# Optimization experiments

Hardware: AMD Instinct MI355X
Metric: run time of the kernel (lower is better)

Reference implementation:

```python
import jax, jax.numpy as jnp
import numpy as np

B, HIST, N, E = 16, 24, 256, 4096
AQI_EM, RNN_H, GNN_H, EDGE_H = 16, 64, 64, 2


def _lstm(x, W_ih, W_hh, b_ih, b_hh):
    # x: [Bn, L, in]; PyTorch LSTM cell, gate order i,f,g,o
    Bn, L, _ = x.shape
    H = W_hh.shape[1]
    xg = jnp.einsum('bli,gi->blg', x, W_ih) + b_ih  # precompute input contributions [Bn,L,4H]

    def step(carry, g_t):
        h, c = carry
        gates = g_t + h @ W_hh.T + b_hh
        i, f, g, o = jnp.split(gates, 4, axis=-1)
        c = jax.nn.sigmoid(f) * c + jax.nn.sigmoid(i) * jnp.tanh(g)
        h = jax.nn.sigmoid(o) * jnp.tanh(c)
        return (h, c), h

    init = (jnp.zeros((Bn, H), x.dtype), jnp.zeros((Bn, H), x.dtype))
    _, hs = jax.lax.scan(step, init, jnp.swapaxes(xg, 0, 1))
    return jnp.swapaxes(hs, 0, 1)  # [Bn,L,H]


def setup_inputs() -> dict:
    key = jax.random.key(0)
    ks = jax.random.split(key, 8)
    return {
        'city_aqi': jax.random.normal(ks[0], (B, HIST, N, 1), jnp.float32),
        'city_conn': jax.random.randint(ks[1], (2, E), 0, N, jnp.int32),
        'city_w': jax.random.normal(ks[2], (E, EDGE_H), jnp.float32),
        'embed_W': jax.random.normal(ks[3], (1, AQI_EM), jnp.float32) * 0.5,
        'embed_b': jnp.zeros((AQI_EM,), jnp.float32),
        'W_ih': jax.random.normal(ks[4], (4 * RNN_H, AQI_EM), jnp.float32) * (1.0 / np.sqrt(RNN_H)),
        'W_hh': jax.random.normal(ks[5], (4 * RNN_H, RNN_H), jnp.float32) * (1.0 / np.sqrt(RNN_H)),
        'b_ih': jnp.zeros((4 * RNN_H,), jnp.float32),
        'b_hh': jnp.zeros((4 * RNN_H,), jnp.float32),
        'mlp1_W': jax.random.normal(ks[6], (2 * RNN_H + EDGE_H, GNN_H), jnp.float32) * (1.0 / np.sqrt(2 * RNN_H + EDGE_H)),
        'mlp1_b': jnp.zeros((GNN_H,), jnp.float32),
        'mlp2_W': jax.random.normal(ks[7], (RNN_H + GNN_H, GNN_H), jnp.float32) * (1.0 / np.sqrt(RNN_H + GNN_H)),
        'mlp2_b': jnp.zeros((GNN_H,), jnp.float32),
        'city_num': N,
    }


def reference(city_aqi, city_conn, city_w, embed_W, embed_b, W_ih, W_hh, b_ih, b_hh, mlp1_W, mlp1_b, mlp2_W, mlp2_b, city_num):
    Bq, L, Nn, _ = city_aqi.shape
    # embedding + LSTM front-end
    x = jnp.transpose(city_aqi, (0, 2, 1, 3))          # [B,N,L,1]
    x = x @ embed_W + embed_b                          # [B,N,L,em]
    x = x.reshape(Bq * Nn, L, -1)
    h = _lstm(x, W_ih, W_hh, b_ih, b_hh)               # [B*N,L,H]
    h = jnp.transpose(h.reshape(Bq, Nn, L, -1), (0, 2, 1, 3))  # [B,L,N,H]
    # batched graph: T = B*L independent graphs with identical edge structure
    T = Bq * L
    x_flat = h.reshape(T * Nn, -1)                     # [T*N,H]
    off = jnp.arange(T, dtype=city_conn.dtype) * jnp.asarray(city_num, city_conn.dtype)
    row = (city_conn[0][None, :] + off[:, None]).reshape(-1)  # [T*E]
    col = (city_conn[1][None, :] + off[:, None]).reshape(-1)
    e = city_conn.shape[1]
    edge_attr = jnp.broadcast_to(city_w[None], (T, e, city_w.shape[1])).reshape(T * e, -1)
    # CityGNN: gather -> concat -> Linear -> scatter_mean -> concat -> Linear
    msg = jnp.concatenate([x_flat[row], x_flat[col], edge_attr], axis=1)
    msg = msg @ mlp1_W + mlp1_b                        # [T*E,gnn_h]
    agg = jax.ops.segment_sum(msg, col, num_segments=T * Nn)
    cnt = jax.ops.segment_sum(jnp.ones((T * e,), msg.dtype), col, num_segments=T * Nn)
    agg = agg / jnp.maximum(cnt, 1.0)[:, None]         # scatter_mean semantics
    out = jnp.concatenate([x_flat, agg], axis=1) @ mlp2_W + mlp2_b
    return out.reshape(-1, L, Nn, out.shape[-1])       # [B,hist_len,N,gnn_h]
```

## Files before the change

### kernel.cpp

```cpp
#include <hip/hip_runtime.h>
#include <hip/hip_bf16.h>

#define B_ 16
#define L_ 24
#define N_ 256
#define E_ 4096
#define T_ (B_ * L_)

constexpr int WP    = 0;
constexpr int WRQ   = WP + 4096;
constexpr int WRM   = WRQ + 4096;
constexpr int WBIAS = WRM + 4096;
constexpr int WALPHA= WBIAS + 16384;
constexpr int WBETA = WALPHA + 256;
constexpr int WDINV = WBETA + 256;
constexpr int WSEL  = WDINV + 256;
constexpr int WSW   = WSEL + 256;
constexpr int WCNTF = WSW + 512;
constexpr int WCOLP = WCNTF + 256;
constexpr int WROWS = WCOLP + 260;
constexpr int WHFRAG= WROWS + 4096;
constexpr int WQFRAG= WHFRAG + 8192;
constexpr int WX    = WQFRAG + 4096;
constexpr int WAFRG = WX + 3145728;

using bf16x8 = __attribute__((ext_vector_type(8))) short;
using f32x4  = __attribute__((ext_vector_type(4))) float;

__device__ __forceinline__ float rcp_(float x) { return __builtin_amdgcn_rcpf(x); }
__device__ __forceinline__ float sigm(float x) { return rcp_(1.f + __expf(-x)); }
__device__ __forceinline__ float tanh_(float x) {
    return fmaf(2.f, rcp_(1.f + __expf(-2.f * x)), -1.f);
}
__device__ __forceinline__ unsigned f2bf(float f) {
    unsigned u = __float_as_uint(f);
    return (u + 0x7fffu + ((u >> 16) & 1u)) >> 16;
}

constexpr int HS = 72;

__global__ __launch_bounds__(256, 1) void k_main(
    const float* __restrict__ aqi, const int* __restrict__ conn,
    const float* __restrict__ cw, const float* __restrict__ Wih,
    const float* __restrict__ embW, const float* __restrict__ embB,
    const float* __restrict__ bih, const float* __restrict__ bhh,
    const float* __restrict__ Whh, const float* __restrict__ m1W,
    const float* __restrict__ m1b, const float* __restrict__ m2W,
    const float* __restrict__ m2b, float* __restrict__ ws) {
    __shared__ __align__(16) char smem[65536];
    int t = threadIdx.x, blk = blockIdx.x;

    if (blk >= 256) {
        int role = blk - 256;
        if (role == 0) {
            int* s_cnt   = (int*)smem;
            float* s_sw0 = (float*)(smem + 1024);
            float* s_sw1 = (float*)(smem + 2048);
            float* sU    = (float*)(smem + 3072);
            s_cnt[t] = 0; s_sw0[t] = 0.f; s_sw1[t] = 0.f;
            __syncthreads();
            for (int e = t; e < E_; e += 256) {
                int c = conn[E_ + e] & 255;
                atomicAdd(&s_cnt[c], 1);
                atomicAdd(&s_sw0[c], cw[2 * e]);
                atomicAdd(&s_sw1[c], cw[2 * e + 1]);
            }
            __syncthreads();
            int cnt = s_cnt[t];
            ws[WCNTF + t] = (float)cnt;
            ws[WDINV + t] = 1.f / (float)(cnt > 1 ? cnt : 1);
            ws[WSEL + t]  = cnt > 0 ? 1.f : 0.f;
            ws[WSW + t]        = s_sw0[t];
            ws[WSW + N_ + t]   = s_sw1[t];
            if (t < 192) {
                int part = t >> 6, j = t & 63;
                float acc = 0.f;
                #pragma unroll 8
                for (int m = 0; m < 64; ++m) {
                    float w = (part == 0) ? m1W[128 * 64 + m]
                            : (part == 1) ? m1W[129 * 64 + m] : m1b[m];
                    acc = fmaf(w, m2W[(64 + m) * 64 + j], acc);
                }
                sU[part * 64 + j] = acc;
            }
            __syncthreads();
            {
                int j = t & 63;
                float u0 = sU[j], u1 = sU[64 + j], u2 = sU[128 + j];
                float b2j = m2b[j];
                int vb = t >> 6;
                #pragma unroll 8
                for (int i = 0; i < 64; ++i) {
                    int v = vb + i * 4;
                    int cv = s_cnt[v];
                    float dv = 1.f / (float)(cv > 1 ? cv : 1);
                    float bb = s_sw0[v] * u0 + s_sw1[v] * u1 + (float)cv * u2;
                    ws[WBIAS + v * 64 + j] = dv * bb + b2j;
                }
            }
            return;
        }
        if (role <= 4) {
            float* sB = (float*)smem;
            float* sM = (float*)(smem + 16384);
            int mi = role - 1;
            bool isP = mi < 2;
            int ks = mi & 1;
            #pragma unroll
            for (int i = 0; i < 16; ++i) sB[t + 256 * i] = m2W[64 * 64 + t + 256 * i];
            __syncthreads();
            int j = t & 63, kl = t >> 6;
            for (int r = 0; r < 8; ++r) {
                int kk = kl * 8 + r;
                int k = ks * 32 + kk;
                const float* arow = m1W + (isP ? k : (64 + k)) * 64;
                float acc = 0.f;
                #pragma unroll
                for (int m = 0; m < 64; m += 4) {
                    float4 a4 = *(const float4*)(arow + m);
                    acc = fmaf(a4.x, sB[m * 64 + j], acc);
                    acc = fmaf(a4.y, sB[(m + 1) * 64 + j], acc);
                    acc = fmaf(a4.z, sB[(m + 2) * 64 + j], acc);
                    acc = fmaf(a4.w, sB[(m + 3) * 64 + j], acc);
                }
                if (isP) {
                    sM[kk * 64 + j] = acc;
                } else {
                    ws[WRM + k * 64 + j] = acc;
                    sM[kk * 64 + j] = acc + m2W[k * 64 + j];
                }
            }
            __syncthreads();
            {
                int ct = t >> 6, l = t & 63;
                int fi = (isP ? 8 : 0) + ks * 4 + ct;
                int rb = (l >> 4) * 8;
                int n = ct * 16 + (l & 15);
                unsigned uu[4];
                #pragma unroll
                for (int q = 0; q < 4; ++q)
                    uu[q] = f2bf(sM[(rb + 2 * q) * 64 + n])
                          | (f2bf(sM[(rb + 2 * q + 1) * 64 + n]) << 16);
                ((uint4*)(ws + WQFRAG))[fi * 64 + l] = make_uint4(uu[0], uu[1], uu[2], uu[3]);
            }
            return;
        }
        unsigned* Mw = (unsigned*)smem;
        for (int i = t; i < 256 * 64; i += 256) Mw[i] = 0u;
        __syncthreads();
        for (int e = t; e < E_; e += 256) {
            int k = conn[e] & 255;
            int v = conn[E_ + e] & 255;
            atomicAdd(&Mw[v * 64 + (k >> 2)], 1u << ((k & 3) * 8));
        }
        __syncthreads();
        uint4* dst = (uint4*)(ws + WAFRG);
        int base = (role - 5) * 2048;
        #pragma unroll
        for (int u0 = 0; u0 < 8; ++u0) {
            int u = base + u0 * 256 + t;
            int fi = u >> 6, l = u & 63;
            int nt = fi >> 3, ks = fi & 7;
            int v = nt * 16 + (l & 15);
            int kb = ks * 8 + ((l >> 4) << 1);
            unsigned w0 = Mw[v * 64 + kb];
            unsigned w1 = Mw[v * 64 + kb + 1];
            unsigned uu[4];
            #pragma unroll
            for (int q = 0; q < 2; ++q) {
                unsigned c0 = (w0 >> (q * 16)) & 255u;
                unsigned c1 = (w0 >> (q * 16 + 8)) & 255u;
                uu[q] = f2bf((float)c0) | (f2bf((float)c1) << 16);
                unsigned d0 = (w1 >> (q * 16)) & 255u;
                unsigned d1 = (w1 >> (q * 16 + 8)) & 255u;
                uu[2 + q] = f2bf((float)d0) | (f2bf((float)d1) << 16);
            }
            dst[u] = make_uint4(uu[0], uu[1], uu[2], uu[3]);
        }
        return;
    }

    short* sHhi = (short*)smem;
    short* sHlo = (short*)(smem + 4608);
    float* sX   = (float*)(smem + 9216);
    int w = t >> 6, lane = t & 63;
    int seq0 = blk * 16;
    int b0 = seq0 >> 8, n0 = seq0 & 255;
    int c0 = lane & 15, quad = lane >> 4, q4 = quad * 4, q8 = quad * 8;
    bf16x8 wreg[4][2];
    #pragma unroll
    for (int g = 0; g < 4; ++g) {
        int ct = 4 * g + w;
        #pragma unroll
        for (int ks = 0; ks < 2; ++ks) {
            const float* src = Whh + (ct * 16 + c0) * 64 + ks * 32 + q8;
            union { bf16x8 v; unsigned u[4]; } tmp;
            #pragma unroll
            for (int q = 0; q < 4; ++q)
                tmp.u[q] = f2bf(src[2 * q]) | (f2bf(src[2 * q + 1]) << 16);
            wreg[g][ks] = tmp.v;
        }
    }
    for (int i = t; i < 384; i += 256) {
        int l = i >> 4, c = i & 15;
        sX[l * 16 + c] = aqi[(b0 * L_ + l) * N_ + n0 + c];
    }
    float alF[4][4], beF[4][4];
    #pragma unroll
    for (int g = 0; g < 4; ++g) {
        #pragma unroll
        for (int r = 0; r < 4; ++r) {
            int tp = (4 * g + w) * 16 + q4 + r;
            float a = 0.f, b = 0.f;
            #pragma unroll
            for (int i = 0; i < 16; ++i) {
                float wv = Wih[tp * 16 + i];
                a += wv * embW[i];
                b += wv * embB[i];
            }
            alF[g][r] = a;
            beF[g][r] = b + bih[tp] + bhh[tp];
        }
    }
    unsigned short* xws = (unsigned short*)(ws + WX);
    float cst[4] = {0.f, 0.f, 0.f, 0.f};
    bf16x8 hA[2][2] = {};
    __syncthreads();
    for (int l = 0; l < L_; ++l) {
        int buf = l & 1;
        float xv = sX[l * 16 + c0];
        f32x4 acc[4];
        #pragma unroll
        for (int g = 0; g < 4; ++g) {
            #pragma unroll
            for (int r = 0; r < 4; ++r)
                acc[g][r] = fmaf(xv, alF[g][r], beF[g][r]);
        }
        if (l > 0) {
            #pragma unroll
            for (int g = 0; g < 4; ++g) {
                #pragma unroll
                for (int ks = 0; ks < 2; ++ks) {
                    acc[g] = __builtin_amdgcn_mfma_f32_16x16x32_bf16(
                        wreg[g][ks], hA[0][ks], acc[g], 0, 0, 0);
                    acc[g] = __builtin_amdgcn_mfma_f32_16x16x32_bf16(
                        wreg[g][ks], hA[1][ks], acc[g], 0, 0, 0);
                }
            }
        }
        unsigned hb[4], lb[4];
        #pragma unroll
        for (int r = 0; r < 4; ++r) {
            float iv = sigm(acc[0][r]);
            float fv = sigm(acc[1][r]);
            float gv = tanh_(acc[2][r]);
            float ov = sigm(acc[3][r]);
            cst[r] = fmaf(fv, cst[r], iv * gv);
            float h = ov * tanh_(cst[r]);
            hb[r] = f2bf(h);
            float hf = __uint_as_float(hb[r] << 16);
            lb[r] = f2bf(h - hf);
        }
        uint2 hw = make_uint2(hb[0] | (hb[1] << 16), hb[2] | (hb[3] << 16));
        uint2 lw = make_uint2(lb[0] | (lb[1] << 16), lb[2] | (lb[3] << 16));
        *(uint2*)&sHhi[buf * (16 * HS) + c0 * HS + w * 16 + q4] = hw;
        *(uint2*)&sHlo[buf * (16 * HS) + c0 * HS + w * 16 + q4] = lw;
        *(uint2*)(xws + ((size_t)(b0 * L_ + l) * N_ + n0) * 64
                  + c0 * 64 + w * 16 + q4) = hw;
        asm volatile("s_waitcnt lgkmcnt(0)" ::: "memory");
        __builtin_amdgcn_s_barrier();
        hA[0][0] = *(const bf16x8*)&sHhi[buf * (16 * HS) + c0 * HS + q8];
        hA[0][1] = *(const bf16x8*)&sHhi[buf * (16 * HS) + c0 * HS + 32 + q8];
        hA[1][0] = *(const bf16x8*)&sHlo[buf * (16 * HS) + c0 * HS + q8];
        hA[1][1] = *(const bf16x8*)&sHlo[buf * (16 * HS) + c0 * HS + 32 + q8];
    }
}

constexpr int XS = 72;

__global__ __launch_bounds__(256, 2) void k_graph(
    const float* __restrict__ ws, float* __restrict__ out) {
    __shared__ __align__(16) short Xl[N_ * XS];
    __shared__ __align__(16) short Sl[N_ * XS];
    int tg = blockIdx.x;
    int tid = threadIdx.x;
    int lane = tid & 63, w = tid >> 6;
    int c0 = lane & 15, quad = lane >> 4, q8 = quad * 8;
    const uint4* src = (const uint4*)((const unsigned short*)(ws + WX)
                                      + (size_t)tg * (N_ * 64));
    #pragma unroll
    for (int it = 0; it < 8; ++it) {
        int idx = tid + it * 256;
        uint4 d = src[idx];
        int node = idx >> 3, q = idx & 7;
        *(uint4*)&Xl[node * XS + q * 8] = d;
    }
    float dv[16];
    #pragma unroll
    for (int nt = 0; nt < 16; ++nt) dv[nt] = ws[WDINV + nt * 16 + c0];
    __syncthreads();
    bf16x8 af[8];
    {
        int colb = w * 16 + (c0 & 14);
        int sh = (c0 & 1) * 16;
        int rbase = (lane >> 4) * 8;
        #pragma unroll
        for (int ks = 0; ks < 8; ++ks) {
            unsigned wd[8];
            #pragma unroll
            for (int j = 0; j < 8; ++j)
                wd[j] = *(const unsigned*)&Xl[(ks * 32 + rbase + j) * XS + colb];
            union { bf16x8 v; unsigned u[4]; } tmp;
            #pragma unroll
            for (int q = 0; q < 4; ++q)
                tmp.u[q] = ((wd[2 * q] >> sh) & 0xffffu)
                         | (((wd[2 * q + 1] >> sh) & 0xffffu) << 16);
            af[ks] = tmp.v;
        }
    }
    f32x4 acc[16];
    #pragma unroll
    for (int nt = 0; nt < 16; ++nt) {
        #pragma unroll
        for (int r = 0; r < 4; ++r) acc[nt][r] = 0.f;
    }
    {
        const bf16x8* bsrc = (const bf16x8*)(ws + WAFRG);
        #pragma unroll
        for (int nt = 0; nt < 16; ++nt) {
            bf16x8 bf[8];
            #pragma unroll
            for (int ks = 0; ks < 8; ++ks)
                bf[ks] = bsrc[(nt * 8 + ks) * 64 + lane];
            #pragma unroll
            for (int ks = 0; ks < 8; ++ks)
                acc[nt] = __builtin_amdgcn_mfma_f32_16x16x32_bf16(
                    af[ks], bf[ks], acc[nt], 0, 0, 0);
        }
    }
    {
        int j0 = w * 16 + quad * 4;
        #pragma unroll
        for (int nt = 0; nt < 16; ++nt) {
            float d = dv[nt];
            unsigned p0 = f2bf(acc[nt][0] * d) | (f2bf(acc[nt][1] * d) << 16);
            unsigned p1 = f2bf(acc[nt][2] * d) | (f2bf(acc[nt][3] * d) << 16);
            int v = nt * 16 + c0;
            *(uint2*)&Sl[v * XS + j0] = make_uint2(p0, p1);
        }
    }
    __syncthreads();
    bf16x8 bq[16];
    {
        const bf16x8* qf = (const bf16x8*)(ws + WQFRAG);
        #pragma unroll
        for (int i = 0; i < 16; ++i) bq[i] = qf[i * 64 + lane];
    }
    const float* bias = ws + WBIAS;
    #pragma unroll
    for (int rti = 0; rti < 4; ++rti) {
        int rt = w * 4 + rti;
        const short* xr = &Xl[(rt * 16 + c0) * XS];
        const short* sr = &Sl[(rt * 16 + c0) * XS];
        bf16x8 ax0 = *(const bf16x8*)(xr + q8);
        bf16x8 ax1 = *(const bf16x8*)(xr + 32 + q8);
        bf16x8 as0 = *(const bf16x8*)(sr + q8);
        bf16x8 as1 = *(const bf16x8*)(sr + 32 + q8);
        #pragma unroll
        for (int ct = 0; ct < 4; ++ct) {
            f32x4 a2;
            #pragma unroll
            for (int r = 0; r < 4; ++r)
                a2[r] = bias[(rt * 16 + quad * 4 + r) * 64 + ct * 16 + c0];
            a2 = __builtin_amdgcn_mfma_f32_16x16x32_bf16(ax0, bq[ct],      a2, 0, 0, 0);
            a2 = __builtin_amdgcn_mfma_f32_16x16x32_bf16(ax1, bq[4 + ct],  a2, 0, 0, 0);
            a2 = __builtin_amdgcn_mfma_f32_16x16x32_bf16(as0, bq[8 + ct],  a2, 0, 0, 0);
            a2 = __builtin_amdgcn_mfma_f32_16x16x32_bf16(as1, bq[12 + ct], a2, 0, 0, 0);
            #pragma unroll
            for (int r = 0; r < 4; ++r)
                out[((size_t)tg * 256 + rt * 16 + quad * 4 + r) * 64 + ct * 16 + c0]
                    = a2[r];
        }
    }
    int v = tid;
    float sel = ws[WSEL + v];
    if (__syncthreads_or(sel < 0.5f)) {
        if (sel < 0.5f) {
            float* og = out + ((size_t)tg * 256 + v) * 64;
            #pragma unroll
            for (int jc = 0; jc < 4; ++jc) {
                float corr[16];
                #pragma unroll
                for (int j = 0; j < 16; ++j) corr[j] = 0.f;
                #pragma unroll
                for (int k = 0; k < 64; ++k) {
                    unsigned hv = (unsigned short)Xl[v * XS + k];
                    float xk = __uint_as_float(hv << 16);
                    const float* Q = ws + WRM + k * 64 + jc * 16;
                    #pragma unroll
                    for (int j = 0; j < 16; ++j) corr[j] += xk * Q[j];
                }
                #pragma unroll
                for (int j = 0; j < 16; ++j) og[jc * 16 + j] -= corr[j];
            }
        }
    }
}

extern "C" void kernel_launch(void* const* d_in, const int* in_sizes, int n_in,
                              void* d_out, int out_size, void* d_ws, size_t ws_size,
                              hipStream_t stream) {
    const float* aqi  = (const float*)d_in[0];
    const int*   conn = (const int*)d_in[1];
    const float* cw   = (const float*)d_in[2];
    const float* embW = (const float*)d_in[3];
    const float* embB = (const float*)d_in[4];
    const float* Wih  = (const float*)d_in[5];
    const float* Whh  = (const float*)d_in[6];
    const float* bih  = (const float*)d_in[7];
    const float* bhh  = (const float*)d_in[8];
    const float* m1W  = (const float*)d_in[9];
    const float* m1b  = (const float*)d_in[10];
    const float* m2W  = (const float*)d_in[11];
    const float* m2b  = (const float*)d_in[12];
    float* ws  = (float*)d_ws;
    float* out = (float*)d_out;

    k_main<<<dim3(265), dim3(256), 0, stream>>>(aqi, conn, cw, Wih, embW, embB,
                                                bih, bhh, Whh, m1W, m1b, m2W,
                                                m2b, ws);
    k_graph<<<dim3(T_), dim3(256), 0, stream>>>(ws, out);
}
```

Measured before the change: 134.8 us.

## Process two 16-sequence LSTM tiles per block with interleaved recurrences

```diff
diff --git a/kernel.cpp b/kernel.cpp
--- a/kernel.cpp
+++ b/kernel.cpp
@@ -38,6 +38,7 @@
 }
 
 constexpr int HS = 72;
+constexpr int NLSTM = 128;
 
 __global__ __launch_bounds__(256, 1) void k_main(
     const float* __restrict__ aqi, const int* __restrict__ conn,
@@ -50,8 +51,8 @@
     __shared__ __align__(16) char smem[65536];
     int t = threadIdx.x, blk = blockIdx.x;
 
-    if (blk >= 256) {
-        int role = blk - 256;
+    if (blk >= NLSTM) {
+        int role = blk - NLSTM;
         if (role == 0) {
             int* s_cnt   = (int*)smem;
             float* s_sw0 = (float*)(smem + 1024);
@@ -180,11 +181,13 @@
         return;
     }
 
-    short* sHhi = (short*)smem;
-    short* sHlo = (short*)(smem + 4608);
-    float* sX   = (float*)(smem + 9216);
+    short* sHhiA = (short*)smem;
+    short* sHloA = (short*)(smem + 4608);
+    short* sHhiB = (short*)(smem + 9216);
+    short* sHloB = (short*)(smem + 13824);
+    float* sX    = (float*)(smem + 18432);
     int w = t >> 6, lane = t & 63;
-    int seq0 = blk * 16;
+    int seq0 = blk * 32;
     int b0 = seq0 >> 8, n0 = seq0 & 255;
     int c0 = lane & 15, quad = lane >> 4, q4 = quad * 4, q8 = quad * 8;
     bf16x8 wreg[4][2];
@@ -201,9 +204,9 @@
             wreg[g][ks] = tmp.v;
         }
     }
-    for (int i = t; i < 384; i += 256) {
-        int l = i >> 4, c = i & 15;
-        sX[l * 16 + c] = aqi[(b0 * L_ + l) * N_ + n0 + c];
+    for (int i = t; i < 768; i += 256) {
+        int l = i >> 5, c = i & 31;
+        sX[l * 32 + c] = aqi[(b0 * L_ + l) * N_ + n0 + c];
     }
     float alF[4][4], beF[4][4];
     #pragma unroll
@@ -223,56 +226,98 @@
         }
     }
     unsigned short* xws = (unsigned short*)(ws + WX);
-    float cst[4] = {0.f, 0.f, 0.f, 0.f};
-    bf16x8 hA[2][2] = {};
+    float cstA[4] = {0.f, 0.f, 0.f, 0.f};
+    float cstB[4] = {0.f, 0.f, 0.f, 0.f};
+    bf16x8 hAa[2][2] = {};
+    bf16x8 hAb[2][2] = {};
     __syncthreads();
     for (int l = 0; l < L_; ++l) {
         int buf = l & 1;
-        float xv = sX[l * 16 + c0];
-        f32x4 acc[4];
+        float xvA = sX[l * 32 + c0];
+        float xvB = sX[l * 32 + 16 + c0];
+        f32x4 accA[4], accB[4];
         #pragma unroll
         for (int g = 0; g < 4; ++g) {
             #pragma unroll
-            for (int r = 0; r < 4; ++r)
-                acc[g][r] = fmaf(xv, alF[g][r], beF[g][r]);
+            for (int r = 0; r < 4; ++r) {
+                accA[g][r] = fmaf(xvA, alF[g][r], beF[g][r]);
+                accB[g][r] = fmaf(xvB, alF[g][r], beF[g][r]);
+            }
         }
         if (l > 0) {
             #pragma unroll
             for (int g = 0; g < 4; ++g) {
                 #pragma unroll
                 for (int ks = 0; ks < 2; ++ks) {
-                    acc[g] = __builtin_amdgcn_mfma_f32_16x16x32_bf16(
-                        wreg[g][ks], hA[0][ks], acc[g], 0, 0, 0);
-                    acc[g] = __builtin_amdgcn_mfma_f32_16x16x32_bf16(
-                        wreg[g][ks], hA[1][ks], acc[g], 0, 0, 0);
-                }
-            }
-        }
-        unsigned hb[4], lb[4];
-        #pragma unroll
-        for (int r = 0; r < 4; ++r) {
-            float iv = sigm(acc[0][r]);
-            float fv = sigm(acc[1][r]);
-            float gv = tanh_(acc[2][r]);
-            float ov = sigm(acc[3][r]);
-            cst[r] = fmaf(fv, cst[r], iv * gv);
-            float h = ov * tanh_(cst[r]);
-            hb[r] = f2bf(h);
-            float hf = __uint_as_float(hb[r] << 16);
-            lb[r] = f2bf(h - hf);
-        }
-        uint2 hw = make_uint2(hb[0] | (hb[1] << 16), hb[2] | (hb[3] << 16));
-        uint2 lw = make_uint2(lb[0] | (lb[1] << 16), lb[2] | (lb[3] << 16));
-        *(uint2*)&sHhi[buf * (16 * HS) + c0 * HS + w * 16 + q4] = hw;
-        *(uint2*)&sHlo[buf * (16 * HS) + c0 * HS + w * 16 + q4] = lw;
-        *(uint2*)(xws + ((size_t)(b0 * L_ + l) * N_ + n0) * 64
-                  + c0 * 64 + w * 16 + q4) = hw;
+                    accA[g] = __builtin_amdgcn_mfma_f32_16x16x32_bf16(
+                        wreg[g][ks], hAa[0][ks], accA[g], 0, 0, 0);
+                    accA[g] = __builtin_amdgcn_mfma_f32_16x16x32_bf16(
+                        wreg[g][ks], hAa[1][ks], accA[g], 0, 0, 0);
+                }
+            }
+            #pragma unroll
+            for (int g = 0; g < 4; ++g) {
+                #pragma unroll
+                for (int ks = 0; ks < 2; ++ks) {
+                    accB[g] = __builtin_amdgcn_mfma_f32_16x16x32_bf16(
+                        wreg[g][ks], hAb[0][ks], accB[g], 0, 0, 0);
+                    accB[g] = __builtin_amdgcn_mfma_f32_16x16x32_bf16(
+                        wreg[g][ks], hAb[1][ks], accB[g], 0, 0, 0);
+                }
+            }
+        }
+        {
+            unsigned hb[4], lb[4];
+            #pragma unroll
+            for (int r = 0; r < 4; ++r) {
+                float iv = sigm(accA[0][r]);
+                float fv = sigm(accA[1][r]);
+                float gv = tanh_(accA[2][r]);
+                float ov = sigm(accA[3][r]);
+                cstA[r] = fmaf(fv, cstA[r], iv * gv);
+                float h = ov * tanh_(cstA[r]);
+                hb[r] = f2bf(h);
+                float hf = __uint_as_float(hb[r] << 16);
+                lb[r] = f2bf(h - hf);
+            }
+            uint2 hw = make_uint2(hb[0] | (hb[1] << 16), hb[2] | (hb[3] << 16));
+            uint2 lw = make_uint2(lb[0] | (lb[1] << 16), lb[2] | (lb[3] << 16));
+            *(uint2*)&sHhiA[buf * (16 * HS) + c0 * HS + w * 16 + q4] = hw;
+            *(uint2*)&sHloA[buf * (16 * HS) + c0 * HS + w * 16 + q4] = lw;
+            *(uint2*)(xws + ((size_t)(b0 * L_ + l) * N_ + n0) * 64
+                      + c0 * 64 + w * 16 + q4) = hw;
+        }
+        {
+            unsigned hb[4], lb[4];
+            #pragma unroll
+            for (int r = 0; r < 4; ++r) {
+                float iv = sigm(accB[0][r]);
+                float fv = sigm(accB[1][r]);
+                float gv = tanh_(accB[2][r]);
+                float ov = sigm(accB[3][r]);
+                cstB[r] = fmaf(fv, cstB[r], iv * gv);
+                float h = ov * tanh_(cstB[r]);
+                hb[r] = f2bf(h);
+                float hf = __uint_as_float(hb[r] << 16);
+                lb[r] = f2bf(h - hf);
+            }
+            uint2 hw = make_uint2(hb[0] | (hb[1] << 16), hb[2] | (hb[3] << 16));
+            uint2 lw = make_uint2(lb[0] | (lb[1] << 16), lb[2] | (lb[3] << 16));
+            *(uint2*)&sHhiB[buf * (16 * HS) + c0 * HS + w * 16 + q4] = hw;
+            *(uint2*)&sHloB[buf * (16 * HS) + c0 * HS + w * 16 + q4] = lw;
+            *(uint2*)(xws + ((size_t)(b0 * L_ + l) * N_ + n0 + 16) * 64
+                      + c0 * 64 + w * 16 + q4) = hw;
+        }
         asm volatile("s_waitcnt lgkmcnt(0)" ::: "memory");
         __builtin_amdgcn_s_barrier();
-        hA[0][0] = *(const bf16x8*)&sHhi[buf * (16 * HS) + c0 * HS + q8];
-        hA[0][1] = *(const bf16x8*)&sHhi[buf * (16 * HS) + c0 * HS + 32 + q8];
-        hA[1][0] = *(const bf16x8*)&sHlo[buf * (16 * HS) + c0 * HS + q8];
-        hA[1][1] = *(const bf16x8*)&sHlo[buf * (16 * HS) + c0 * HS + 32 + q8];
+        hAa[0][0] = *(const bf16x8*)&sHhiA[buf * (16 * HS) + c0 * HS + q8];
+        hAa[0][1] = *(const bf16x8*)&sHhiA[buf * (16 * HS) + c0 * HS + 32 + q8];
+        hAa[1][0] = *(const bf16x8*)&sHloA[buf * (16 * HS) + c0 * HS + q8];
+        hAa[1][1] = *(const bf16x8*)&sHloA[buf * (16 * HS) + c0 * HS + 32 + q8];
+        hAb[0][0] = *(const bf16x8*)&sHhiB[buf * (16 * HS) + c0 * HS + q8];
+        hAb[0][1] = *(const bf16x8*)&sHhiB[buf * (16 * HS) + c0 * HS + 32 + q8];
+        hAb[1][0] = *(const bf16x8*)&sHloB[buf * (16 * HS) + c0 * HS + q8];
+        hAb[1][1] = *(const bf16x8*)&sHloB[buf * (16 * HS) + c0 * HS + 32 + q8];
     }
 }
 
@@ -426,8 +471,8 @@
     float* ws  = (float*)d_ws;
     float* out = (float*)d_out;
 
-    k_main<<<dim3(265), dim3(256), 0, stream>>>(aqi, conn, cw, Wih, embW, embB,
-                                                bih, bhh, Whh, m1W, m1b, m2W,
-                                                m2b, ws);
+    k_main<<<dim3(NLSTM + 9), dim3(256), 0, stream>>>(aqi, conn, cw, Wih, embW,
+                                                      embB, bih, bhh, Whh, m1W,
+                                                      m1b, m2W, m2b, ws);
     k_graph<<<dim3(T_), dim3(256), 0, stream>>>(ws, out);
 }
```

After: 143.4 us. 1.06x slower.

## Pack two LSTM sequence groups per 512-thread block to halve LSTM block count

Applied to the files above, without the earlier changes.

```diff
diff --git a/kernel.cpp b/kernel.cpp
--- a/kernel.cpp
+++ b/kernel.cpp
@@ -38,8 +38,9 @@
 }
 
 constexpr int HS = 72;
-
-__global__ __launch_bounds__(256, 1) void k_main(
+constexpr int NLSTM = 128;
+
+__global__ __launch_bounds__(512, 1) void k_main(
     const float* __restrict__ aqi, const int* __restrict__ conn,
     const float* __restrict__ cw, const float* __restrict__ Wih,
     const float* __restrict__ embW, const float* __restrict__ embB,
@@ -50,28 +51,30 @@
     __shared__ __align__(16) char smem[65536];
     int t = threadIdx.x, blk = blockIdx.x;
 
-    if (blk >= 256) {
-        int role = blk - 256;
+    if (blk >= NLSTM) {
+        int role = blk - NLSTM;
         if (role == 0) {
             int* s_cnt   = (int*)smem;
             float* s_sw0 = (float*)(smem + 1024);
             float* s_sw1 = (float*)(smem + 2048);
             float* sU    = (float*)(smem + 3072);
-            s_cnt[t] = 0; s_sw0[t] = 0.f; s_sw1[t] = 0.f;
+            if (t < 256) { s_cnt[t] = 0; s_sw0[t] = 0.f; s_sw1[t] = 0.f; }
             __syncthreads();
-            for (int e = t; e < E_; e += 256) {
+            for (int e = t; e < E_; e += 512) {
                 int c = conn[E_ + e] & 255;
                 atomicAdd(&s_cnt[c], 1);
                 atomicAdd(&s_sw0[c], cw[2 * e]);
                 atomicAdd(&s_sw1[c], cw[2 * e + 1]);
             }
             __syncthreads();
-            int cnt = s_cnt[t];
-            ws[WCNTF + t] = (float)cnt;
-            ws[WDINV + t] = 1.f / (float)(cnt > 1 ? cnt : 1);
-            ws[WSEL + t]  = cnt > 0 ? 1.f : 0.f;
-            ws[WSW + t]        = s_sw0[t];
-            ws[WSW + N_ + t]   = s_sw1[t];
+            if (t < 256) {
+                int cnt = s_cnt[t];
+                ws[WCNTF + t] = (float)cnt;
+                ws[WDINV + t] = 1.f / (float)(cnt > 1 ? cnt : 1);
+                ws[WSEL + t]  = cnt > 0 ? 1.f : 0.f;
+                ws[WSW + t]        = s_sw0[t];
+                ws[WSW + N_ + t]   = s_sw1[t];
+            }
             if (t < 192) {
                 int part = t >> 6, j = t & 63;
                 float acc = 0.f;
@@ -90,8 +93,8 @@
                 float b2j = m2b[j];
                 int vb = t >> 6;
                 #pragma unroll 8
-                for (int i = 0; i < 64; ++i) {
-                    int v = vb + i * 4;
+                for (int i = 0; i < 32; ++i) {
+                    int v = vb + i * 8;
                     int cv = s_cnt[v];
                     float dv = 1.f / (float)(cv > 1 ? cv : 1);
                     float bb = s_sw0[v] * u0 + s_sw1[v] * u1 + (float)cv * u2;
@@ -107,11 +110,11 @@
             bool isP = mi < 2;
             int ks = mi & 1;
             #pragma unroll
-            for (int i = 0; i < 16; ++i) sB[t + 256 * i] = m2W[64 * 64 + t + 256 * i];
+            for (int i = 0; i < 8; ++i) sB[t + 512 * i] = m2W[64 * 64 + t + 512 * i];
             __syncthreads();
             int j = t & 63, kl = t >> 6;
-            for (int r = 0; r < 8; ++r) {
-                int kk = kl * 8 + r;
+            for (int r = 0; r < 4; ++r) {
+                int kk = kl * 4 + r;
                 int k = ks * 32 + kk;
                 const float* arow = m1W + (isP ? k : (64 + k)) * 64;
                 float acc = 0.f;
@@ -131,7 +134,7 @@
                 }
             }
             __syncthreads();
-            {
+            if (t < 256) {
                 int ct = t >> 6, l = t & 63;
                 int fi = (isP ? 8 : 0) + ks * 4 + ct;
                 int rb = (l >> 4) * 8;
@@ -146,9 +149,9 @@
             return;
         }
         unsigned* Mw = (unsigned*)smem;
-        for (int i = t; i < 256 * 64; i += 256) Mw[i] = 0u;
+        for (int i = t; i < 256 * 64; i += 512) Mw[i] = 0u;
         __syncthreads();
-        for (int e = t; e < E_; e += 256) {
+        for (int e = t; e < E_; e += 512) {
             int k = conn[e] & 255;
             int v = conn[E_ + e] & 255;
             atomicAdd(&Mw[v * 64 + (k >> 2)], 1u << ((k & 3) * 8));
@@ -157,8 +160,8 @@
         uint4* dst = (uint4*)(ws + WAFRG);
         int base = (role - 5) * 2048;
         #pragma unroll
-        for (int u0 = 0; u0 < 8; ++u0) {
-            int u = base + u0 * 256 + t;
+        for (int u0 = 0; u0 < 4; ++u0) {
+            int u = base + u0 * 512 + t;
             int fi = u >> 6, l = u & 63;
             int nt = fi >> 3, ks = fi & 7;
             int v = nt * 16 + (l & 15);
@@ -180,17 +183,18 @@
         return;
     }
 
-    short* sHhi = (short*)smem;
-    short* sHlo = (short*)(smem + 4608);
-    float* sX   = (float*)(smem + 9216);
     int w = t >> 6, lane = t & 63;
-    int seq0 = blk * 16;
+    int grp = w >> 2, wg = w & 3;
+    short* sHhi = (short*)(smem + grp * 9216);
+    short* sHlo = (short*)(smem + grp * 9216 + 4608);
+    float* sX   = (float*)(smem + 18432);
+    int seq0 = blk * 32 + grp * 16;
     int b0 = seq0 >> 8, n0 = seq0 & 255;
     int c0 = lane & 15, quad = lane >> 4, q4 = quad * 4, q8 = quad * 8;
     bf16x8 wreg[4][2];
     #pragma unroll
     for (int g = 0; g < 4; ++g) {
-        int ct = 4 * g + w;
+        int ct = 4 * g + wg;
         #pragma unroll
         for (int ks = 0; ks < 2; ++ks) {
             const float* src = Whh + (ct * 16 + c0) * 64 + ks * 32 + q8;
@@ -201,16 +205,19 @@
             wreg[g][ks] = tmp.v;
         }
     }
-    for (int i = t; i < 384; i += 256) {
-        int l = i >> 4, c = i & 15;
-        sX[l * 16 + c] = aqi[(b0 * L_ + l) * N_ + n0 + c];
+    {
+        int sb0 = (blk * 32) >> 8, sn0 = (blk * 32) & 255;
+        for (int i = t; i < 768; i += 512) {
+            int l = i >> 5, c = i & 31;
+            sX[l * 32 + c] = aqi[(sb0 * L_ + l) * N_ + sn0 + c];
+        }
     }
     float alF[4][4], beF[4][4];
     #pragma unroll
     for (int g = 0; g < 4; ++g) {
         #pragma unroll
         for (int r = 0; r < 4; ++r) {
-            int tp = (4 * g + w) * 16 + q4 + r;
+            int tp = (4 * g + wg) * 16 + q4 + r;
             float a = 0.f, b = 0.f;
             #pragma unroll
             for (int i = 0; i < 16; ++i) {
@@ -228,7 +235,7 @@
     __syncthreads();
     for (int l = 0; l < L_; ++l) {
         int buf = l & 1;
-        float xv = sX[l * 16 + c0];
+        float xv = sX[l * 32 + grp * 16 + c0];
         f32x4 acc[4];
         #pragma unroll
         for (int g = 0; g < 4; ++g) {
@@ -263,10 +270,10 @@
         }
         uint2 hw = make_uint2(hb[0] | (hb[1] << 16), hb[2] | (hb[3] << 16));
         uint2 lw = make_uint2(lb[0] | (lb[1] << 16), lb[2] | (lb[3] << 16));
-        *(uint2*)&sHhi[buf * (16 * HS) + c0 * HS + w * 16 + q4] = hw;
-        *(uint2*)&sHlo[buf * (16 * HS) + c0 * HS + w * 16 + q4] = lw;
+        *(uint2*)&sHhi[buf * (16 * HS) + c0 * HS + wg * 16 + q4] = hw;
+        *(uint2*)&sHlo[buf * (16 * HS) + c0 * HS + wg * 16 + q4] = lw;
         *(uint2*)(xws + ((size_t)(b0 * L_ + l) * N_ + n0) * 64
-                  + c0 * 64 + w * 16 + q4) = hw;
+                  + c0 * 64 + wg * 16 + q4) = hw;
         asm volatile("s_waitcnt lgkmcnt(0)" ::: "memory");
         __builtin_amdgcn_s_barrier();
         hA[0][0] = *(const bf16x8*)&sHhi[buf * (16 * HS) + c0 * HS + q8];
@@ -426,8 +433,8 @@
     float* ws  = (float*)d_ws;
     float* out = (float*)d_out;
 
-    k_main<<<dim3(265), dim3(256), 0, stream>>>(aqi, conn, cw, Wih, embW, embB,
-                                                bih, bhh, Whh, m1W, m1b, m2W,
-                                                m2b, ws);
+    k_main<<<dim3(NLSTM + 9), dim3(512), 0, stream>>>(aqi, conn, cw, Wih, embW,
+                                                      embB, bih, bhh, Whh, m1W,
+                                                      m1b, m2W, m2b, ws);
     k_graph<<<dim3(T_), dim3(256), 0, stream>>>(ws, out);
 }
```

Measured after the change: 142.9 us. +6.0%, slower.
